# Kernel tuning notes

Measured on AMD Instinct MI355X. Metric: run time of the kernel, lower is better.

Reference implementation:

```python
import jax, jax.numpy as jnp
import numpy as np

B, NF, EMB = 2048, 32, 64
FEAT_MAP_DIM = [128, 128, 128]  # split_half=True, activation=None


def setup_inputs() -> dict:
    key = jax.random.key(0)
    ks = jax.random.split(key, 7)
    inp = jax.random.normal(ks[0], (B, NF, EMB), dtype=jnp.float32)
    # conv1d_i: in_channels = H_{i-1} * NF, out_channels = FEAT_MAP_DIM[i]
    # H_0 = NF = 32; H_1 = H_2 = 128 // 2 = 64 (split_half)
    in_chs = [NF * NF, (FEAT_MAP_DIM[0] // 2) * NF, (FEAT_MAP_DIM[1] // 2) * NF]
    params = {}
    for i, (ic, oc) in enumerate(zip(in_chs, FEAT_MAP_DIM)):
        bound = 1.0 / np.sqrt(ic)  # torch Conv1d default init range
        params[f"W{i}"] = jax.random.uniform(ks[1 + 2 * i], (oc, ic), jnp.float32, -bound, bound)
        params[f"b{i}"] = jax.random.uniform(ks[2 + 2 * i], (oc,), jnp.float32, -bound, bound)
    return {"inp": inp, **params}


def reference(inp, W0, b0, W1, b1, W2, b2):
    # CIN: h_k[b,o,e] = sum_{j,z} W_k[o, j*NF+z] * h_{k-1}[b,j,e] * inp[b,z,e] + b_k[o]
    # The torch code materializes the outer product then applies a 1x1 conv;
    # the fused triple einsum below computes identical math.
    nf = inp.shape[1]
    Ws, bs = [W0, W1, W2], [b0, b1, b2]
    h = inp
    outs = []
    n_layers = len(Ws)
    for i, (W, b) in enumerate(zip(Ws, bs)):
        O, Hj = W.shape[0], h.shape[1]
        Wr = W.reshape(O, Hj, nf)  # channel index c = j*nf + z
        nxt = jnp.einsum('bjk,bzk,ojz->bok', h, inp, Wr) + b[None, :, None]
        if i != n_layers - 1:  # split_half
            h, o = nxt[:, : O // 2], nxt[:, O // 2 :]
        else:
            o = nxt
        outs.append(o)
    out = jnp.concatenate(outs, axis=1)  # (B, 64+64+128, EMB)
    return jnp.sum(out, axis=2)  # (B, 256)
```

## Files before the change

### kernel.cpp

```cpp
#include <hip/hip_runtime.h>


typedef _Float16 f16;
typedef _Float16 f16x4 __attribute__((ext_vector_type(4)));
typedef _Float16 f16x8 __attribute__((ext_vector_type(8)));
typedef float f32x4 __attribute__((ext_vector_type(4)));
typedef float f32x16 __attribute__((ext_vector_type(16)));

#define HSTR 72
#define GSTR 163840
#define P0G  0
#define P1G  32768
#define P2G  98304

__device__ __forceinline__ f32x16 zero16() {
    f32x16 v;
#pragma unroll
    for (int i = 0; i < 16; ++i) v[i] = 0.0f;
    return v;
}

__global__ void __launch_bounds__(256)
prep_frag(const float* __restrict__ W0, const float* __restrict__ W1,
          const float* __restrict__ W2, f16* __restrict__ dst)
{
    int g = (blockIdx.x * 256 + threadIdx.x) * 8;
    const float* src; int base, KK, rbase;
    if (g < 65536)       { src = W0; base = 0;      KK = 64;  rbase = 0;  }
    else if (g < 131072) { src = W0; base = 65536;  KK = 64;  rbase = 64; }
    else if (g < 262144) { src = W1; base = 131072; KK = 128; rbase = 0;  }
    else if (g < 393216) { src = W1; base = 262144; KK = 128; rbase = 64; }
    else                 { src = W2; base = 393216; KK = 128; rbase = 0;  }
    int local = g - base;
    int frag  = local >> 9;
    int lane  = (local >> 3) & 63;
    int kk    = frag % KK;
    int mc    = frag / KK;
    int row   = rbase + mc * 32 + (lane & 31);
    int col   = kk * 16 + (lane >> 5) * 8;
    int IC    = KK * 16;
    const float* s = src + (size_t)row * IC + col;
    f16x8 o;
#pragma unroll
    for (int i = 0; i < 8; ++i) o[i] = (f16)s[i];
    *(f16x8*)(dst + g) = o;
}

__device__ __forceinline__ void p_chunk(const f16* __restrict__ hrows,
                                        const f16x8 (&pB)[4],
                                        f16* __restrict__ pdst, int jb,
                                        int t, int q)
{
    f32x16 acc = zero16();
#pragma unroll
    for (int s = 0; s < 4; ++s) {
        f16x8 a = *(const f16x8*)(hrows + t * HSTR + s * 16 + q * 8);
        acc = __builtin_amdgcn_mfma_f32_32x32x16_f16(a, pB[s], acc, 0, 0, 0);
    }
#pragma unroll
    for (int r = 0; r < 16; ++r) {
        int j = jb + (r & 3) + 8 * (r >> 2) + 4 * q;
        int f = j * 2 + (t >> 4);
        pdst[f * 512 + ((t >> 3) & 1) * 256 + (t & 7)] = (f16)acc[r];
    }
}

template <int HJ>
__device__ __forceinline__ void h_gemm4(const f16* __restrict__ Hf,
                                        const f16* __restrict__ h0,
                                        const f16* __restrict__ h1,
                                        int lane8, int t,
                                        const f16x8 (&ip)[2][2][2],
                                        f32x16 (&acc)[2][2])
{
    acc[0][0] = zero16(); acc[0][1] = zero16();
    acc[1][0] = zero16(); acc[1][1] = zero16();
    const f16* Wp = Hf + lane8;
    f16x8 wf[2][2];
    f16   sc[2][4];
#pragma unroll
    for (int ph = 0; ph < 2; ++ph) {
        wf[ph][0] = *(const f16x8*)(Wp + (ph * 2 + 0) * 512);
        wf[ph][1] = *(const f16x8*)(Wp + (ph * 2 + 1) * 512);
        sc[ph][0] = h0[ph * HSTR + t];
        sc[ph][1] = h0[ph * HSTR + 32 + t];
        sc[ph][2] = h1[ph * HSTR + t];
        sc[ph][3] = h1[ph * HSTR + 32 + t];
    }
    for (int jj = 0; jj < HJ; jj += 2) {
#pragma unroll
        for (int ph = 0; ph < 2; ++ph) {
            f16x8 w0 = wf[ph][0], w1 = wf[ph][1];
            f16 s00 = sc[ph][0], s01 = sc[ph][1];
            f16 s10 = sc[ph][2], s11 = sc[ph][3];
            int jn = jj + ph + 2;
            if (jn > HJ - 1) jn = HJ - 1;
            wf[ph][0] = *(const f16x8*)(Wp + (jn * 2 + 0) * 512);
            wf[ph][1] = *(const f16x8*)(Wp + (jn * 2 + 1) * 512);
            sc[ph][0] = h0[jn * HSTR + t];
            sc[ph][1] = h0[jn * HSTR + 32 + t];
            sc[ph][2] = h1[jn * HSTR + t];
            sc[ph][3] = h1[jn * HSTR + 32 + t];
            acc[0][0] = __builtin_amdgcn_mfma_f32_32x32x16_f16(w0, ip[0][0][0] * s00, acc[0][0], 0, 0, 0);
            acc[0][0] = __builtin_amdgcn_mfma_f32_32x32x16_f16(w1, ip[0][1][0] * s00, acc[0][0], 0, 0, 0);
            acc[0][1] = __builtin_amdgcn_mfma_f32_32x32x16_f16(w0, ip[0][0][1] * s01, acc[0][1], 0, 0, 0);
            acc[0][1] = __builtin_amdgcn_mfma_f32_32x32x16_f16(w1, ip[0][1][1] * s01, acc[0][1], 0, 0, 0);
            acc[1][0] = __builtin_amdgcn_mfma_f32_32x32x16_f16(w0, ip[1][0][0] * s10, acc[1][0], 0, 0, 0);
            acc[1][0] = __builtin_amdgcn_mfma_f32_32x32x16_f16(w1, ip[1][1][0] * s10, acc[1][0], 0, 0, 0);
            acc[1][1] = __builtin_amdgcn_mfma_f32_32x32x16_f16(w0, ip[1][0][1] * s11, acc[1][1], 0, 0, 0);
            acc[1][1] = __builtin_amdgcn_mfma_f32_32x32x16_f16(w1, ip[1][1][1] * s11, acc[1][1], 0, 0, 0);
        }
    }
}

__device__ __forceinline__ void load_bias(const float* __restrict__ bl,
                                          float (&bve)[16], int g, int q)
{
#pragma unroll
    for (int r = 0; r < 16; ++r)
        bve[r] = bl[g * 32 + (r & 3) + 8 * (r >> 2) + 4 * q];
}

__device__ __forceinline__ void epi4(const f32x16 (&acc)[2][2],
                                     f16* __restrict__ h0d, f16* __restrict__ h1d,
                                     const float (&bve)[16], int g, int t, int q)
{
#pragma unroll
    for (int r = 0; r < 16; ++r) {
        int row = g * 32 + (r & 3) + 8 * (r >> 2) + 4 * q;
        h0d[row * HSTR + t]      = (f16)(acc[0][0][r] + bve[r]);
        h0d[row * HSTR + 32 + t] = (f16)(acc[0][1][r] + bve[r]);
        h1d[row * HSTR + t]      = (f16)(acc[1][0][r] + bve[r]);
        h1d[row * HSTR + 32 + t] = (f16)(acc[1][1][r] + bve[r]);
    }
}

__global__ void __launch_bounds__(256, 2)
cin_h(const float* __restrict__ inp, const f16* __restrict__ Wf,
      f16* __restrict__ pW,
      const float* __restrict__ b0v, const float* __restrict__ b1v)
{
    __shared__ __attribute__((aligned(16))) f16 hL[4 * 64 * HSTR];

    const int tid   = threadIdx.x;
    const int w     = tid >> 6;
    const int lane  = tid & 63;
    const int t     = lane & 31;
    const int q     = lane >> 5;
    const int lane8 = lane * 8;
    const int bp    = w & 1;
    const int g     = w >> 1;
    const int b0i   = blockIdx.x * 4;

#pragma unroll
    for (int it = 0; it < 8; ++it) {
        int idx = it * 1024 + tid * 4;
        int b = idx >> 11, rem = idx & 2047;
        int z = rem >> 6, k = rem & 63;
        f32x4 v = *(const f32x4*)(inp + (size_t)(b0i + b) * 2048 + rem);
        f16x4 h4;
        h4[0] = (f16)v[0]; h4[1] = (f16)v[1]; h4[2] = (f16)v[2]; h4[3] = (f16)v[3];
        *(f16x4*)(hL + b * 64 * HSTR + z * HSTR + k) = h4;
    }
    __syncthreads();

    f16x8 ip[2][2][2];
#pragma unroll
    for (int b = 0; b < 2; ++b) {
        const f16* src = hL + (bp * 2 + b) * 64 * HSTR;
#pragma unroll
        for (int kq = 0; kq < 2; ++kq)
#pragma unroll
            for (int nh = 0; nh < 2; ++nh) {
                f16x8 v;
#pragma unroll
                for (int i = 0; i < 8; ++i)
                    v[i] = src[(kq * 16 + q * 8 + i) * HSTR + nh * 32 + t];
                ip[b][kq][nh] = v;
            }
    }
    f16x8 pB[4];
#pragma unroll
    for (int s = 0; s < 4; ++s)
        pB[s] = *(const f16x8*)(hL + w * 64 * HSTR + t * HSTR + s * 16 + q * 8);

    const int bglob = b0i + w;
    f16* pG = pW + (size_t)(bglob >> 5) * GSTR + (bglob & 31) * 8;
    const f16* H0 = Wf;
    const f16* H1 = Wf + 131072;
    f16* hA = hL + (bp * 2) * 64 * HSTR;
    f16* hB = hL + (bp * 2 + 1) * 64 * HSTR;
    f32x16 acc[2][2];
    float bve[16];

    p_chunk(hL + w * 64 * HSTR, pB, pG + P0G, 0, t, q);
    h_gemm4<32>(H0 + g * 64 * 512, hA, hB, lane8, t, ip, acc);
    load_bias(b0v, bve, g, q);
    __syncthreads();
    epi4(acc, hA, hB, bve, g, t, q);
    __syncthreads();

    p_chunk(hL + w * 64 * HSTR,             pB, pG + P1G, 0,  t, q);
    p_chunk(hL + w * 64 * HSTR + 32 * HSTR, pB, pG + P1G, 32, t, q);
    h_gemm4<64>(H1 + g * 128 * 512, hA, hB, lane8, t, ip, acc);
    load_bias(b1v, bve, g, q);
    __syncthreads();
    epi4(acc, hA, hB, bve, g, t, q);
    __syncthreads();

    p_chunk(hL + w * 64 * HSTR,             pB, pG + P2G, 0,  t, q);
    p_chunk(hL + w * 64 * HSTR + 32 * HSTR, pB, pG + P2G, 32, t, q);
}

template <int KK>
__device__ __forceinline__ void o_tile(const f16* __restrict__ Of,
                                       const f16* __restrict__ pBase,
                                       const float* __restrict__ biasp,
                                       float* __restrict__ out,
                                       float* __restrict__ rP,
                                       int bg, int colbase, int tid)
{
    const int w = tid >> 6, lane = tid & 63, t = lane & 31, q = lane >> 5;
    const int lane8 = lane * 8;
    const int mi = w & 1, ki = w >> 1;
    const int SQ = KK / 8;
    const f16* Ap = Of + (size_t)(mi * KK + ki * SQ) * 512 + lane8;
    const f16* Bp = pBase + (size_t)(ki * SQ) * 512 + lane8;

    f32x16 acc = zero16();
    f16x8 af[8], bf[8];
#pragma unroll
    for (int i = 0; i < 8; ++i) {
        af[i] = *(const f16x8*)(Ap + i * 512);
        bf[i] = *(const f16x8*)(Bp + i * 512);
    }
#pragma unroll 8
    for (int s = 0; s < SQ; ++s) {
        int idx = s & 7;
        f16x8 a = af[idx], b = bf[idx];
        int sn = s + 8 < SQ ? s + 8 : SQ - 1;
        af[idx] = *(const f16x8*)(Ap + sn * 512);
        bf[idx] = *(const f16x8*)(Bp + sn * 512);
        acc = __builtin_amdgcn_mfma_f32_32x32x16_f16(a, b, acc, 0, 0, 0);
    }
#pragma unroll
    for (int r = 0; r < 16; ++r) {
        int m = mi * 32 + (r & 3) + 8 * (r >> 2) + 4 * q;
        rP[(ki * 32 + t) * 64 + m] = acc[r];
    }
    __syncthreads();
    {
        int n = tid >> 5;
        int o = (tid & 31) * 2;
        float v0 = 0.0f, v1 = 0.0f;
#pragma unroll
        for (int k2 = 0; k2 < 8; ++k2) {
            v0 += rP[(k2 * 32 + n) * 64 + o];
            v1 += rP[(k2 * 32 + n) * 64 + o + 1];
        }
        float* op = out + (size_t)(bg * 32 + n) * 256 + colbase + o;
        op[0] = v0 + 64.0f * biasp[o];
        op[1] = v1 + 64.0f * biasp[o + 1];
    }
}

__global__ void __launch_bounds__(1024, 1)
cin_out(const f16* __restrict__ Wf, const f16* __restrict__ pW,
        const float* __restrict__ b0v, const float* __restrict__ b1v,
        const float* __restrict__ b2v, float* __restrict__ out)
{
    __shared__ __attribute__((aligned(16))) float rP[8 * 32 * 64];
    const int tid = threadIdx.x;
    const int r  = blockIdx.x & 3;
    const int bg = blockIdx.x >> 2;
    const f16* pGrp = pW + (size_t)bg * GSTR;
    if (r == 0)
        o_tile<64> (Wf + 65536,  pGrp + P0G, b0v + 64, out, rP, bg, 0,   tid);
    else if (r == 1)
        o_tile<128>(Wf + 262144, pGrp + P1G, b1v + 64, out, rP, bg, 64,  tid);
    else if (r == 2)
        o_tile<128>(Wf + 393216, pGrp + P2G, b2v,      out, rP, bg, 128, tid);
    else
        o_tile<128>(Wf + 524288, pGrp + P2G, b2v + 64, out, rP, bg, 192, tid);
}

extern "C" void kernel_launch(void* const* d_in, const int* in_sizes, int n_in,
                              void* d_out, int out_size, void* d_ws, size_t ws_size,
                              hipStream_t stream)
{
    const float* inp = (const float*)d_in[0];
    const float* W0  = (const float*)d_in[1];
    const float* b0  = (const float*)d_in[2];
    const float* W1  = (const float*)d_in[3];
    const float* b1  = (const float*)d_in[4];
    const float* W2  = (const float*)d_in[5];
    const float* b2  = (const float*)d_in[6];
    float* out = (float*)d_out;

    f16* Wf = (f16*)d_ws;
    f16* pW = Wf + 655360;

    prep_frag<<<320, 256, 0, stream>>>(W0, W1, W2, Wf);
    cin_h<<<512, 256, 0, stream>>>(inp, Wf, pW, b0, b1);
    cin_out<<<256, 1024, 0, stream>>>(Wf, pW, b0, b1, b2, out);
}
```

Before: 132.3 us.

## Fuse output reduction into cin_h using shared-memory pooled features and fdot2 matvec

Removes the cin_out kernel and the global pW intermediate: the pooled outer-product sums are kept in shared memory, and each block computes its output columns with packed fp16 dot products (fdot2) against the output-weight fragments, then reduces across waves in LDS. This avoids writing and re-reading the large pW buffer and one kernel launch. In exchange, each block streams the full output weight matrices from global or L2 for only 4 batch rows using non-MFMA ALU work. That raises weight traffic and ALU load per block, and the larger shared-memory footprint may reduce occupancy.

After: 140.5 us. 6.2% more time.

```diff
diff --git a/kernel.cpp b/kernel.cpp
--- a/kernel.cpp
+++ b/kernel.cpp
@@ -2,16 +2,16 @@
 
 
 typedef _Float16 f16;
+typedef _Float16 f16x2 __attribute__((ext_vector_type(2)));
 typedef _Float16 f16x4 __attribute__((ext_vector_type(4)));
 typedef _Float16 f16x8 __attribute__((ext_vector_type(8)));
 typedef float f32x4 __attribute__((ext_vector_type(4)));
 typedef float f32x16 __attribute__((ext_vector_type(16)));
 
 #define HSTR 72
-#define GSTR 163840
-#define P0G  0
-#define P1G  32768
-#define P2G  98304
+#define HB   4608
+#define P0O  18432
+#define P1O  22528
 
 __device__ __forceinline__ f32x16 zero16() {
     f32x16 v;
@@ -60,8 +60,7 @@
 #pragma unroll
     for (int r = 0; r < 16; ++r) {
         int j = jb + (r & 3) + 8 * (r >> 2) + 4 * q;
-        int f = j * 2 + (t >> 4);
-        pdst[f * 512 + ((t >> 3) & 1) * 256 + (t & 7)] = (f16)acc[r];
+        pdst[j * 32 + t] = (f16)acc[r];
     }
 }
 
@@ -135,12 +134,52 @@
     }
 }
 
+template <int KK, int MC, int KKQ>
+__device__ __forceinline__ void mv_region(const f16* __restrict__ Of,
+                                          const f16* __restrict__ pL, int pStride,
+                                          int kk0, int lane,
+                                          float (&acc)[4][8], int rgb)
+{
+    const int half8 = (lane >> 5) * 8;
+    const f16* Wp = Of + lane * 8;
+#pragma unroll 2
+    for (int kk = kk0; kk < kk0 + KKQ; ++kk) {
+        f16x8 ps[4];
+#pragma unroll
+        for (int b = 0; b < 4; ++b)
+            ps[b] = *(const f16x8*)(pL + b * pStride + kk * 16 + half8);
+#pragma unroll
+        for (int mc = 0; mc < MC; ++mc) {
+            f16x8 wf = *(const f16x8*)(Wp + (size_t)(mc * KK + kk) * 512);
+#pragma unroll
+            for (int b = 0; b < 4; ++b) {
+#if __has_builtin(__builtin_amdgcn_fdot2)
+                const f16x2* w2 = (const f16x2*)&wf;
+                const f16x2* p2 = (const f16x2*)&ps[b];
+                float a = acc[b][rgb + mc];
+                a = __builtin_amdgcn_fdot2(w2[0], p2[0], a, false);
+                a = __builtin_amdgcn_fdot2(w2[1], p2[1], a, false);
+                a = __builtin_amdgcn_fdot2(w2[2], p2[2], a, false);
+                a = __builtin_amdgcn_fdot2(w2[3], p2[3], a, false);
+                acc[b][rgb + mc] = a;
+#else
+                float a = acc[b][rgb + mc];
+#pragma unroll
+                for (int i = 0; i < 8; ++i)
+                    a = fmaf((float)wf[i], (float)ps[b][i], a);
+                acc[b][rgb + mc] = a;
+#endif
+            }
+        }
+    }
+}
+
 __global__ void __launch_bounds__(256, 2)
 cin_h(const float* __restrict__ inp, const f16* __restrict__ Wf,
-      f16* __restrict__ pW,
-      const float* __restrict__ b0v, const float* __restrict__ b1v)
-{
-    __shared__ __attribute__((aligned(16))) f16 hL[4 * 64 * HSTR];
+      const float* __restrict__ b0v, const float* __restrict__ b1v,
+      const float* __restrict__ b2v, float* __restrict__ out)
+{
+    __shared__ __attribute__((aligned(16))) f16 smem[30720];
 
     const int tid   = threadIdx.x;
     const int w     = tid >> 6;
@@ -151,6 +190,7 @@
     const int bp    = w & 1;
     const int g     = w >> 1;
     const int b0i   = blockIdx.x * 4;
+    f16* hL = smem;
 
 #pragma unroll
     for (int it = 0; it < 8; ++it) {
@@ -160,14 +200,14 @@
         f32x4 v = *(const f32x4*)(inp + (size_t)(b0i + b) * 2048 + rem);
         f16x4 h4;
         h4[0] = (f16)v[0]; h4[1] = (f16)v[1]; h4[2] = (f16)v[2]; h4[3] = (f16)v[3];
-        *(f16x4*)(hL + b * 64 * HSTR + z * HSTR + k) = h4;
+        *(f16x4*)(hL + b * HB + z * HSTR + k) = h4;
     }
     __syncthreads();
 
     f16x8 ip[2][2][2];
 #pragma unroll
     for (int b = 0; b < 2; ++b) {
-        const f16* src = hL + (bp * 2 + b) * 64 * HSTR;
+        const f16* src = hL + (bp * 2 + b) * HB;
 #pragma unroll
         for (int kq = 0; kq < 2; ++kq)
 #pragma unroll
@@ -182,106 +222,77 @@
     f16x8 pB[4];
 #pragma unroll
     for (int s = 0; s < 4; ++s)
-        pB[s] = *(const f16x8*)(hL + w * 64 * HSTR + t * HSTR + s * 16 + q * 8);
-
-    const int bglob = b0i + w;
-    f16* pG = pW + (size_t)(bglob >> 5) * GSTR + (bglob & 31) * 8;
+        pB[s] = *(const f16x8*)(hL + w * HB + t * HSTR + s * 16 + q * 8);
+
     const f16* H0 = Wf;
     const f16* H1 = Wf + 131072;
-    f16* hA = hL + (bp * 2) * 64 * HSTR;
-    f16* hB = hL + (bp * 2 + 1) * 64 * HSTR;
+    f16* hA = hL + (bp * 2) * HB;
+    f16* hB2 = hL + (bp * 2 + 1) * HB;
     f32x16 acc[2][2];
     float bve[16];
 
-    p_chunk(hL + w * 64 * HSTR, pB, pG + P0G, 0, t, q);
-    h_gemm4<32>(H0 + g * 64 * 512, hA, hB, lane8, t, ip, acc);
+    p_chunk(hL + w * HB, pB, smem + P0O + w * 1024, 0, t, q);
+    h_gemm4<32>(H0 + g * 64 * 512, hA, hB2, lane8, t, ip, acc);
     load_bias(b0v, bve, g, q);
     __syncthreads();
-    epi4(acc, hA, hB, bve, g, t, q);
-    __syncthreads();
-
-    p_chunk(hL + w * 64 * HSTR,             pB, pG + P1G, 0,  t, q);
-    p_chunk(hL + w * 64 * HSTR + 32 * HSTR, pB, pG + P1G, 32, t, q);
-    h_gemm4<64>(H1 + g * 128 * 512, hA, hB, lane8, t, ip, acc);
+    epi4(acc, hA, hB2, bve, g, t, q);
+    __syncthreads();
+
+    p_chunk(hL + w * HB,             pB, smem + P1O + w * 2048, 0,  t, q);
+    p_chunk(hL + w * HB + 32 * HSTR, pB, smem + P1O + w * 2048, 32, t, q);
+    h_gemm4<64>(H1 + g * 128 * 512, hA, hB2, lane8, t, ip, acc);
     load_bias(b1v, bve, g, q);
     __syncthreads();
-    epi4(acc, hA, hB, bve, g, t, q);
-    __syncthreads();
-
-    p_chunk(hL + w * 64 * HSTR,             pB, pG + P2G, 0,  t, q);
-    p_chunk(hL + w * 64 * HSTR + 32 * HSTR, pB, pG + P2G, 32, t, q);
-}
-
-template <int KK>
-__device__ __forceinline__ void o_tile(const f16* __restrict__ Of,
-                                       const f16* __restrict__ pBase,
-                                       const float* __restrict__ biasp,
-                                       float* __restrict__ out,
-                                       float* __restrict__ rP,
-                                       int bg, int colbase, int tid)
-{
-    const int w = tid >> 6, lane = tid & 63, t = lane & 31, q = lane >> 5;
-    const int lane8 = lane * 8;
-    const int mi = w & 1, ki = w >> 1;
-    const int SQ = KK / 8;
-    const f16* Ap = Of + (size_t)(mi * KK + ki * SQ) * 512 + lane8;
-    const f16* Bp = pBase + (size_t)(ki * SQ) * 512 + lane8;
-
-    f32x16 acc = zero16();
-    f16x8 af[8], bf[8];
-#pragma unroll
-    for (int i = 0; i < 8; ++i) {
-        af[i] = *(const f16x8*)(Ap + i * 512);
-        bf[i] = *(const f16x8*)(Bp + i * 512);
-    }
-#pragma unroll 8
-    for (int s = 0; s < SQ; ++s) {
-        int idx = s & 7;
-        f16x8 a = af[idx], b = bf[idx];
-        int sn = s + 8 < SQ ? s + 8 : SQ - 1;
-        af[idx] = *(const f16x8*)(Ap + sn * 512);
-        bf[idx] = *(const f16x8*)(Bp + sn * 512);
-        acc = __builtin_amdgcn_mfma_f32_32x32x16_f16(a, b, acc, 0, 0, 0);
-    }
-#pragma unroll
-    for (int r = 0; r < 16; ++r) {
-        int m = mi * 32 + (r & 3) + 8 * (r >> 2) + 4 * q;
-        rP[(ki * 32 + t) * 64 + m] = acc[r];
-    }
-    __syncthreads();
+    epi4(acc, hA, hB2, bve, g, t, q);
+    __syncthreads();
+
+    p_chunk(hL + w * HB,             pB, hL + w * HB, 0,  t, q);
+    p_chunk(hL + w * HB + 32 * HSTR, pB, hL + w * HB, 32, t, q);
+    __syncthreads();
+
     {
-        int n = tid >> 5;
-        int o = (tid & 31) * 2;
-        float v0 = 0.0f, v1 = 0.0f;
-#pragma unroll
-        for (int k2 = 0; k2 < 8; ++k2) {
-            v0 += rP[(k2 * 32 + n) * 64 + o];
-            v1 += rP[(k2 * 32 + n) * 64 + o + 1];
+        float acc8[4][8];
+#pragma unroll
+        for (int b = 0; b < 4; ++b)
+#pragma unroll
+            for (int rg = 0; rg < 8; ++rg) acc8[b][rg] = 0.0f;
+
+        mv_region<64, 2, 16>(Wf + 65536,  smem + P0O, 1024, w * 16, lane, acc8, 0);
+        mv_region<128, 2, 32>(Wf + 262144, smem + P1O, 2048, w * 32, lane, acc8, 2);
+        mv_region<128, 4, 32>(Wf + 393216, hL,         HB,   w * 32, lane, acc8, 4);
+        __syncthreads();
+
+        float* rPf = (float*)smem;
+#pragma unroll
+        for (int b = 0; b < 4; ++b)
+#pragma unroll
+            for (int rg = 0; rg < 8; ++rg)
+                rPf[((w * 4 + b) * 8 + rg) * 64 + lane] = acc8[b][rg];
+    }
+    __syncthreads();
+
+    {
+        const float* rPf = (const float*)smem;
+#pragma unroll
+        for (int it = 0; it < 4; ++it) {
+            int idx = it * 256 + tid;
+            int b   = idx >> 8;
+            int rem = idx & 255;
+            int rg  = rem >> 5;
+            int r32 = rem & 31;
+            float s = 0.0f;
+#pragma unroll
+            for (int wv = 0; wv < 4; ++wv) {
+                s += rPf[((wv * 4 + b) * 8 + rg) * 64 + r32];
+                s += rPf[((wv * 4 + b) * 8 + rg) * 64 + 32 + r32];
+            }
+            int col; float bias;
+            if (rg < 2)      { col = rg * 32 + r32;           bias = b0v[64 + col]; }
+            else if (rg < 4) { col = 64 + (rg - 2) * 32 + r32; bias = b1v[col]; }
+            else             { col = 128 + (rg - 4) * 32 + r32; bias = b2v[col - 128]; }
+            out[(size_t)(b0i + b) * 256 + col] = s + 64.0f * bias;
         }
-        float* op = out + (size_t)(bg * 32 + n) * 256 + colbase + o;
-        op[0] = v0 + 64.0f * biasp[o];
-        op[1] = v1 + 64.0f * biasp[o + 1];
-    }
-}
-
-__global__ void __launch_bounds__(1024, 1)
-cin_out(const f16* __restrict__ Wf, const f16* __restrict__ pW,
-        const float* __restrict__ b0v, const float* __restrict__ b1v,
-        const float* __restrict__ b2v, float* __restrict__ out)
-{
-    __shared__ __attribute__((aligned(16))) float rP[8 * 32 * 64];
-    const int tid = threadIdx.x;
-    const int r  = blockIdx.x & 3;
-    const int bg = blockIdx.x >> 2;
-    const f16* pGrp = pW + (size_t)bg * GSTR;
-    if (r == 0)
-        o_tile<64> (Wf + 65536,  pGrp + P0G, b0v + 64, out, rP, bg, 0,   tid);
-    else if (r == 1)
-        o_tile<128>(Wf + 262144, pGrp + P1G, b1v + 64, out, rP, bg, 64,  tid);
-    else if (r == 2)
-        o_tile<128>(Wf + 393216, pGrp + P2G, b2v,      out, rP, bg, 128, tid);
-    else
-        o_tile<128>(Wf + 524288, pGrp + P2G, b2v + 64, out, rP, bg, 192, tid);
+    }
 }
 
 extern "C" void kernel_launch(void* const* d_in, const int* in_sizes, int n_in,
@@ -298,9 +309,7 @@
     float* out = (float*)d_out;
 
     f16* Wf = (f16*)d_ws;
-    f16* pW = Wf + 655360;
 
     prep_frag<<<320, 256, 0, stream>>>(W0, W1, W2, Wf);
-    cin_h<<<512, 256, 0, stream>>>(inp, Wf, pW, b0, b1);
-    cin_out<<<256, 1024, 0, stream>>>(Wf, pW, b0, b1, b2, out);
-}
+    cin_h<<<512, 256, 0, stream>>>(inp, Wf, b0, b1, b2, out);
+}
```
